# Kernel optimization log

Hardware: AMD Instinct MI355X
Metric: run time of the kernel (lower is better)

The kernel has to match this reference:

```python
import jax, jax.numpy as jnp
import numpy as np

MARGIN = 0.5
TAU = 0.25
RHO = 10.0
SEMIHARD_LOSS_THRESHOLD = 0.0
EPS = 1e-12


def _pairwise_cosine_distances(x):
    # L2-normalize rows, distances = 1 - cosine similarity  -> [N, N]
    xn = x / jnp.maximum(jnp.linalg.norm(x, axis=1, keepdims=True), EPS)
    sim = xn @ xn.T
    dist = 1.0 - sim
    return dist, sim, xn


def _source_similarities(src):
    # distances normalized by their batch mean ('relative' / avg distances)
    dist, sim, xn = _pairwise_cosine_distances(src)
    avg_dist = dist / jnp.maximum(jnp.mean(dist), EPS)
    return dist, avg_dist, sim, xn


def _weights_from_distances(avg_dist, tau):
    # soft relaxed label weights from teacher distances
    pair_weights = jnp.exp(-avg_dist / tau)                      # [N, N] pos-pair weight
    neg_pair_weights = 1.0 - pair_weights                        # [N, N]
    # triplet (i, j=pos, k=neg): weight = w_pos[i,j] * w_neg[i,k]  -> [N, N, N]
    triplet_weights = pair_weights[:, :, None] * neg_pair_weights[:, None, :]
    return pair_weights, neg_pair_weights, triplet_weights


def _safe_division(num, den):
    return jnp.where(den > 0.0, num / jnp.where(den > 0.0, den, 1.0), 0.0)


def setup_inputs() -> dict:
    key = jax.random.key(0)
    k1, k2 = jax.random.split(key)
    N, D = 384, 128
    source_embeddings = jax.random.normal(k1, (N, D), dtype=jnp.float32)
    embeddings = jax.random.normal(k2, (N, D), dtype=jnp.float32)
    return {"source_embeddings": source_embeddings, "embeddings": embeddings}


def reference(source_embeddings, embeddings):
    src = jax.lax.stop_gradient(source_embeddings)  # .detach()
    _, source_avg_distances, _, _ = _source_similarities(src)
    source_pair_weights, _, source_triplet_weights = _weights_from_distances(
        source_avg_distances, TAU)

    distances, _, _ = _pairwise_cosine_distances(embeddings)  # [N, N]
    # tdd[i, j, k] = d[i, k] - d[i, j]
    triplet_distance_differences = distances[:, None, :] - distances[:, :, None]
    triplet_losses = jax.nn.relu(MARGIN - triplet_distance_differences)  # [N, N, N]

    semihard = ((triplet_losses > 0.0) & (triplet_losses <= MARGIN)).astype(
        triplet_losses.dtype) * source_triplet_weights
    positive_pair_semihard_losses = jnp.max(triplet_losses * semihard, axis=2)  # [N, N]

    if SEMIHARD_LOSS_THRESHOLD > 0.0:
        hard = (triplet_losses > MARGIN).astype(triplet_losses.dtype) * source_triplet_weights
        normalized = jnp.min(triplet_losses - RHO * hard, axis=2)
        positive_pair_hard_losses = (normalized + RHO) * (normalized < 0.0).astype(
            normalized.dtype)
    else:
        positive_pair_hard_losses = 0.0

    gate = (positive_pair_semihard_losses <= SEMIHARD_LOSS_THRESHOLD).astype(
        positive_pair_semihard_losses.dtype)
    positive_pair_losses = positive_pair_semihard_losses + gate * positive_pair_hard_losses

    loss = _safe_division(jnp.sum(positive_pair_losses * source_pair_weights),
                          jnp.sum(source_pair_weights))
    return loss
```

## Files before the change

kernel.cpp:

```cpp
#include <hip/hip_runtime.h>
#include <hip/hip_bf16.h>

#define N 384
#define D 128
#define TAU 0.25f
#define MARGIN 0.5f

__global__ __launch_bounds__(64) void k_norm(const float* __restrict__ src,
                                             const float* __restrict__ emb,
                                             float* __restrict__ xn_src,
                                             float* __restrict__ xn_emb,
                                             float* __restrict__ accum) {
    int b = blockIdx.x;
    int lane = threadIdx.x;
    if (b == 0 && lane == 0) { accum[0] = 0.f; accum[1] = 0.f; accum[2] = 0.f; }
    const float* x;
    float* y;
    int row;
    if (b < N) { x = src; y = xn_src; row = b; }
    else       { x = emb; y = xn_emb; row = b - N; }
    float2 v = ((const float2*)(x + (size_t)row * D))[lane];
    float ss = v.x * v.x + v.y * v.y;
    #pragma unroll
    for (int o = 32; o > 0; o >>= 1) ss += __shfl_xor(ss, o);
    float inv = 1.0f / fmaxf(sqrtf(ss), 1e-12f);
    float2 o2 = {v.x * inv, v.y * inv};
    ((float2*)(y + (size_t)row * D))[lane] = o2;
}

__global__ __launch_bounds__(256) void k_gram(const float* __restrict__ xn_src,
                                              const float* __restrict__ xn_emb,
                                              float* __restrict__ dsrc,
                                              float* __restrict__ demb,
                                              float* __restrict__ accum) {
    __shared__ float At[D][34];
    __shared__ float Bt[D][34];
    __shared__ float ps[4];
    int bid = blockIdx.x;
    int mat = (bid >= 144) ? 1 : 0;
    int t2  = mat ? bid - 144 : bid;
    int bi = t2 / 12, bj = t2 % 12;
    const float* xn = mat ? xn_emb : xn_src;
    float* out      = mat ? demb : dsrc;
    int lin = threadIdx.x;
    #pragma unroll
    for (int l = 0; l < 4; l++) {
        int idx = lin + l * 256;
        int row = idx >> 5;
        int c4  = idx & 31;
        float4 va = ((const float4*)(xn + (size_t)(bi * 32 + row) * D))[c4];
        At[c4 * 4 + 0][row] = va.x; At[c4 * 4 + 1][row] = va.y;
        At[c4 * 4 + 2][row] = va.z; At[c4 * 4 + 3][row] = va.w;
        float4 vb = ((const float4*)(xn + (size_t)(bj * 32 + row) * D))[c4];
        Bt[c4 * 4 + 0][row] = vb.x; Bt[c4 * 4 + 1][row] = vb.y;
        Bt[c4 * 4 + 2][row] = vb.z; Bt[c4 * 4 + 3][row] = vb.w;
    }
    __syncthreads();
    int tx = lin & 15, ty = lin >> 4;
    float a00 = 0.f, a01 = 0.f, a10 = 0.f, a11 = 0.f;
    #pragma unroll 8
    for (int k = 0; k < D; k++) {
        float x0 = At[k][2 * ty], x1 = At[k][2 * ty + 1];
        float y0 = Bt[k][2 * tx], y1 = Bt[k][2 * tx + 1];
        a00 = fmaf(x0, y0, a00); a01 = fmaf(x0, y1, a01);
        a10 = fmaf(x1, y0, a10); a11 = fmaf(x1, y1, a11);
    }
    float d00 = 1.f - a00, d01 = 1.f - a01, d10 = 1.f - a10, d11 = 1.f - a11;
    int r0 = bi * 32 + 2 * ty, c0 = bj * 32 + 2 * tx;
    out[(size_t)r0 * N + c0]           = d00;
    out[(size_t)r0 * N + c0 + 1]       = d01;
    out[(size_t)(r0 + 1) * N + c0]     = d10;
    out[(size_t)(r0 + 1) * N + c0 + 1] = d11;
    if (!mat) {
        float s = d00 + d01 + d10 + d11;
        #pragma unroll
        for (int o = 32; o > 0; o >>= 1) s += __shfl_xor(s, o);
        if ((lin & 63) == 0) ps[lin >> 6] = s;
        __syncthreads();
        if (lin == 0) atomicAdd(&accum[0], ps[0] + ps[1] + ps[2] + ps[3]);
    }
}

__global__ __launch_bounds__(256) void k_weights(float* __restrict__ wsrc,
                                                 const float* __restrict__ accum) {
    float mean  = accum[0] * (1.0f / (float)(N * N));
    float scale = 1.0f / (fmaxf(mean, 1e-12f) * TAU);
    int idx = blockIdx.x * 256 + threadIdx.x;
    wsrc[idx] = expf(-wsrc[idx] * scale);
}

__global__ __launch_bounds__(N) void k_main(const float* __restrict__ wp,
                                            const float* __restrict__ de,
                                            float* __restrict__ accum) {
    __shared__ float pn[6], pd[6];
    int i = blockIdx.x;
    int t = threadIdx.x;
    const float* der = de + (size_t)i * N;
    const float* wpr = wp + (size_t)i * N;
    float q = der[t];
    float c = MARGIN + q;
    float m0 = 0.f, m1 = 0.f, m2 = 0.f, m3 = 0.f;
    #pragma unroll 2
    for (int k = 0; k < N; k += 4) {
        float dk0 = der[k], dk1 = der[k + 1], dk2 = der[k + 2], dk3 = der[k + 3];
        float wk0 = wpr[k], wk1 = wpr[k + 1], wk2 = wpr[k + 2], wk3 = wpr[k + 3];
        float tl0 = c - dk0; float v0 = tl0 * (1.f - wk0);
        v0 = (tl0 <= MARGIN) ? v0 : 0.f; m0 = fmaxf(m0, v0);
        float tl1 = c - dk1; float v1 = tl1 * (1.f - wk1);
        v1 = (tl1 <= MARGIN) ? v1 : 0.f; m1 = fmaxf(m1, v1);
        float tl2 = c - dk2; float v2 = tl2 * (1.f - wk2);
        v2 = (tl2 <= MARGIN) ? v2 : 0.f; m2 = fmaxf(m2, v2);
        float tl3 = c - dk3; float v3 = tl3 * (1.f - wk3);
        v3 = (tl3 <= MARGIN) ? v3 : 0.f; m3 = fmaxf(m3, v3);
    }
    float m = fmaxf(fmaxf(m0, m1), fmaxf(m2, m3));
    float w = wpr[t];
    float numc = w * w * m;
    float denc = w;
    #pragma unroll
    for (int o = 32; o > 0; o >>= 1) {
        numc += __shfl_xor(numc, o);
        denc += __shfl_xor(denc, o);
    }
    if ((t & 63) == 0) { pn[t >> 6] = numc; pd[t >> 6] = denc; }
    __syncthreads();
    if (t == 0) {
        float sn = 0.f, sd = 0.f;
        #pragma unroll
        for (int wv = 0; wv < 6; wv++) { sn += pn[wv]; sd += pd[wv]; }
        atomicAdd(&accum[1], sn);
        atomicAdd(&accum[2], sd);
    }
}

__global__ void k_final(const float* __restrict__ accum, float* __restrict__ out) {
    float num = accum[1], den = accum[2];
    out[0] = (den > 0.0f) ? num / den : 0.0f;
}

extern "C" void kernel_launch(void* const* d_in, const int* in_sizes, int n_in,
                              void* d_out, int out_size, void* d_ws, size_t ws_size,
                              hipStream_t stream) {
    const float* src = (const float*)d_in[0];
    const float* emb = (const float*)d_in[1];
    float* out = (float*)d_out;

    float* ws = (float*)d_ws;
    float* xn_src = ws;
    float* xn_emb = xn_src + N * D;
    float* wsrc   = xn_emb + N * D;
    float* demb   = wsrc + N * N;
    float* accum  = demb + N * N;

    k_norm<<<2 * N, 64, 0, stream>>>(src, emb, xn_src, xn_emb, accum);
    k_gram<<<2 * 144, 256, 0, stream>>>(xn_src, xn_emb, wsrc, demb, accum);
    k_weights<<<(N * N) / 256, 256, 0, stream>>>(wsrc, accum);
    k_main<<<N, N, 0, stream>>>(wsrc, demb, accum);
    k_final<<<1, 1, 0, stream>>>(accum, out);
}
```

Baseline: 87.28 us.

## Fuse normalization, weights and final division into two kernels

Row L2 normalization moves into the Gram kernel, where norms are computed per tile and applied while staging into shared memory. The exp weight computation moves into the main kernel, which sums per-block partial distance sums itself. The final division runs in the last block via an atomic ticket counter. This cuts five launches to two and drops intermediate global round-trips, at the cost of redundant norm computation across tiles and a serial 144-element sum in every thread.

```diff
diff --git a/kernel.cpp b/kernel.cpp
--- a/kernel.cpp
+++ b/kernel.cpp
@@ -6,56 +6,57 @@
 #define TAU 0.25f
 #define MARGIN 0.5f
 
-__global__ __launch_bounds__(64) void k_norm(const float* __restrict__ src,
-                                             const float* __restrict__ emb,
-                                             float* __restrict__ xn_src,
-                                             float* __restrict__ xn_emb,
-                                             float* __restrict__ accum) {
-    int b = blockIdx.x;
-    int lane = threadIdx.x;
-    if (b == 0 && lane == 0) { accum[0] = 0.f; accum[1] = 0.f; accum[2] = 0.f; }
-    const float* x;
-    float* y;
-    int row;
-    if (b < N) { x = src; y = xn_src; row = b; }
-    else       { x = emb; y = xn_emb; row = b - N; }
-    float2 v = ((const float2*)(x + (size_t)row * D))[lane];
-    float ss = v.x * v.x + v.y * v.y;
-    #pragma unroll
-    for (int o = 32; o > 0; o >>= 1) ss += __shfl_xor(ss, o);
-    float inv = 1.0f / fmaxf(sqrtf(ss), 1e-12f);
-    float2 o2 = {v.x * inv, v.y * inv};
-    ((float2*)(y + (size_t)row * D))[lane] = o2;
-}
-
-__global__ __launch_bounds__(256) void k_gram(const float* __restrict__ xn_src,
-                                              const float* __restrict__ xn_emb,
+__global__ __launch_bounds__(256) void k_gram(const float* __restrict__ xsrc,
+                                              const float* __restrict__ xemb,
                                               float* __restrict__ dsrc,
                                               float* __restrict__ demb,
+                                              float* __restrict__ tsum,
                                               float* __restrict__ accum) {
     __shared__ float At[D][34];
     __shared__ float Bt[D][34];
+    __shared__ float inv_s[64];
     __shared__ float ps[4];
     int bid = blockIdx.x;
+    int lin = threadIdx.x;
+    if (bid == 0 && lin == 0) {
+        accum[0] = 0.f; accum[1] = 0.f;
+        ((unsigned int*)accum)[2] = 0u;
+    }
     int mat = (bid >= 144) ? 1 : 0;
     int t2  = mat ? bid - 144 : bid;
     int bi = t2 / 12, bj = t2 % 12;
-    const float* xn = mat ? xn_emb : xn_src;
+    const float* xn = mat ? xemb : xsrc;
     float* out      = mat ? demb : dsrc;
-    int lin = threadIdx.x;
+
+    int wv = lin >> 6, lane = lin & 63;
     #pragma unroll
-    for (int l = 0; l < 4; l++) {
+    for (int rr = 0; rr < 16; ++rr) {
+        int vr = wv * 16 + rr;
+        int r  = vr & 31;
+        int grow = ((vr >> 5) ? bj : bi) * 32 + r;
+        float2 v = ((const float2*)(xn + (size_t)grow * D))[lane];
+        float ss = v.x * v.x + v.y * v.y;
+        #pragma unroll
+        for (int o = 32; o > 0; o >>= 1) ss += __shfl_xor(ss, o);
+        if (lane == 0) inv_s[vr] = 1.0f / fmaxf(sqrtf(ss), 1e-12f);
+    }
+    __syncthreads();
+
+    #pragma unroll
+    for (int l = 0; l < 4; ++l) {
         int idx = lin + l * 256;
         int row = idx >> 5;
         int c4  = idx & 31;
+        float ia = inv_s[row], ib = inv_s[32 + row];
         float4 va = ((const float4*)(xn + (size_t)(bi * 32 + row) * D))[c4];
-        At[c4 * 4 + 0][row] = va.x; At[c4 * 4 + 1][row] = va.y;
-        At[c4 * 4 + 2][row] = va.z; At[c4 * 4 + 3][row] = va.w;
+        At[c4 * 4 + 0][row] = va.x * ia; At[c4 * 4 + 1][row] = va.y * ia;
+        At[c4 * 4 + 2][row] = va.z * ia; At[c4 * 4 + 3][row] = va.w * ia;
         float4 vb = ((const float4*)(xn + (size_t)(bj * 32 + row) * D))[c4];
-        Bt[c4 * 4 + 0][row] = vb.x; Bt[c4 * 4 + 1][row] = vb.y;
-        Bt[c4 * 4 + 2][row] = vb.z; Bt[c4 * 4 + 3][row] = vb.w;
+        Bt[c4 * 4 + 0][row] = vb.x * ib; Bt[c4 * 4 + 1][row] = vb.y * ib;
+        Bt[c4 * 4 + 2][row] = vb.z * ib; Bt[c4 * 4 + 3][row] = vb.w * ib;
     }
     __syncthreads();
+
     int tx = lin & 15, ty = lin >> 4;
     float a00 = 0.f, a01 = 0.f, a10 = 0.f, a11 = 0.f;
     #pragma unroll 8
@@ -71,50 +72,52 @@
     out[(size_t)r0 * N + c0 + 1]       = d01;
     out[(size_t)(r0 + 1) * N + c0]     = d10;
     out[(size_t)(r0 + 1) * N + c0 + 1] = d11;
+
     if (!mat) {
         float s = d00 + d01 + d10 + d11;
         #pragma unroll
         for (int o = 32; o > 0; o >>= 1) s += __shfl_xor(s, o);
         if ((lin & 63) == 0) ps[lin >> 6] = s;
         __syncthreads();
-        if (lin == 0) atomicAdd(&accum[0], ps[0] + ps[1] + ps[2] + ps[3]);
+        if (lin == 0) tsum[t2] = ps[0] + ps[1] + ps[2] + ps[3];
     }
 }
 
-__global__ __launch_bounds__(256) void k_weights(float* __restrict__ wsrc,
-                                                 const float* __restrict__ accum) {
-    float mean  = accum[0] * (1.0f / (float)(N * N));
-    float scale = 1.0f / (fmaxf(mean, 1e-12f) * TAU);
-    int idx = blockIdx.x * 256 + threadIdx.x;
-    wsrc[idx] = expf(-wsrc[idx] * scale);
-}
-
-__global__ __launch_bounds__(N) void k_main(const float* __restrict__ wp,
-                                            const float* __restrict__ de,
-                                            float* __restrict__ accum) {
+__global__ __launch_bounds__(N) void k_main(const float* __restrict__ dsrc,
+                                            const float* __restrict__ demb,
+                                            const float* __restrict__ tsum,
+                                            float* __restrict__ accum,
+                                            float* __restrict__ out) {
+    __shared__ float wn[N];
     __shared__ float pn[6], pd[6];
     int i = blockIdx.x;
     int t = threadIdx.x;
-    const float* der = de + (size_t)i * N;
-    const float* wpr = wp + (size_t)i * N;
-    float q = der[t];
-    float c = MARGIN + q;
+    float total = 0.f;
+    #pragma unroll
+    for (int j = 0; j < 144; ++j) total += tsum[j];
+    float mean  = total * (1.0f / (float)(N * N));
+    float scale = 1.0f / (fmaxf(mean, 1e-12f) * TAU);
+    const float* dsr = dsrc + (size_t)i * N;
+    const float* der = demb + (size_t)i * N;
+    float w = expf(-dsr[t] * scale);
+    wn[t] = 1.0f - w;
+    float c = MARGIN + der[t];
+    __syncthreads();
     float m0 = 0.f, m1 = 0.f, m2 = 0.f, m3 = 0.f;
     #pragma unroll 2
     for (int k = 0; k < N; k += 4) {
-        float dk0 = der[k], dk1 = der[k + 1], dk2 = der[k + 2], dk3 = der[k + 3];
-        float wk0 = wpr[k], wk1 = wpr[k + 1], wk2 = wpr[k + 2], wk3 = wpr[k + 3];
-        float tl0 = c - dk0; float v0 = tl0 * (1.f - wk0);
+        float4 wvk = *(const float4*)&wn[k];
+        float d0 = der[k], d1 = der[k + 1], d2 = der[k + 2], d3 = der[k + 3];
+        float tl0 = c - d0; float v0 = tl0 * wvk.x;
         v0 = (tl0 <= MARGIN) ? v0 : 0.f; m0 = fmaxf(m0, v0);
-        float tl1 = c - dk1; float v1 = tl1 * (1.f - wk1);
+        float tl1 = c - d1; float v1 = tl1 * wvk.y;
         v1 = (tl1 <= MARGIN) ? v1 : 0.f; m1 = fmaxf(m1, v1);
-        float tl2 = c - dk2; float v2 = tl2 * (1.f - wk2);
+        float tl2 = c - d2; float v2 = tl2 * wvk.z;
         v2 = (tl2 <= MARGIN) ? v2 : 0.f; m2 = fmaxf(m2, v2);
-        float tl3 = c - dk3; float v3 = tl3 * (1.f - wk3);
+        float tl3 = c - d3; float v3 = tl3 * wvk.w;
         v3 = (tl3 <= MARGIN) ? v3 : 0.f; m3 = fmaxf(m3, v3);
     }
     float m = fmaxf(fmaxf(m0, m1), fmaxf(m2, m3));
-    float w = wpr[t];
     float numc = w * w * m;
     float denc = w;
     #pragma unroll
@@ -128,14 +131,16 @@
         float sn = 0.f, sd = 0.f;
         #pragma unroll
         for (int wv = 0; wv < 6; wv++) { sn += pn[wv]; sd += pd[wv]; }
-        atomicAdd(&accum[1], sn);
-        atomicAdd(&accum[2], sd);
+        atomicAdd(&accum[0], sn);
+        atomicAdd(&accum[1], sd);
+        __threadfence();
+        unsigned int tk = atomicAdd((unsigned int*)accum + 2, 1u);
+        if (tk == (unsigned int)(N - 1)) {
+            float num = atomicAdd(&accum[0], 0.f);
+            float den = atomicAdd(&accum[1], 0.f);
+            out[0] = (den > 0.f) ? num / den : 0.f;
+        }
     }
-}
-
-__global__ void k_final(const float* __restrict__ accum, float* __restrict__ out) {
-    float num = accum[1], den = accum[2];
-    out[0] = (den > 0.0f) ? num / den : 0.0f;
 }
 
 extern "C" void kernel_launch(void* const* d_in, const int* in_sizes, int n_in,
@@ -146,15 +151,11 @@
     float* out = (float*)d_out;
 
     float* ws = (float*)d_ws;
-    float* xn_src = ws;
-    float* xn_emb = xn_src + N * D;
-    float* wsrc   = xn_emb + N * D;
-    float* demb   = wsrc + N * N;
-    float* accum  = demb + N * N;
+    float* dsrc  = ws;
+    float* demb  = dsrc + N * N;
+    float* tsum  = demb + N * N;
+    float* accum = tsum + 144;
 
-    k_norm<<<2 * N, 64, 0, stream>>>(src, emb, xn_src, xn_emb, accum);
-    k_gram<<<2 * 144, 256, 0, stream>>>(xn_src, xn_emb, wsrc, demb, accum);
-    k_weights<<<(N * N) / 256, 256, 0, stream>>>(wsrc, accum);
-    k_main<<<N, N, 0, stream>>>(wsrc, demb, accum);
-    k_final<<<1, 1, 0, stream>>>(accum, out);
+    k_gram<<<288, 256, 0, stream>>>(src, emb, dsrc, demb, tsum, accum);
+    k_main<<<N, N, 0, stream>>>(dsrc, demb, tsum, accum, out);
 }
```

Result: slower. 94.42 us (+8.2%).

## Compute mean distance via column-sum identity and fuse exp into gram kernel

Applied to the files above, without the earlier changes.

Computes the mean source cosine distance algebraically as N^2 minus the squared norm of the summed normalized rows. A small single-block kernel does this before the gram kernel, which lets the exp weight transform be fused into the gram kernel's store and removes the separate weights pass. The final division is folded into the main kernel using a last-block ticket counter, which eliminates the final kernel launch. The net launch count drops from five to four, at the cost of a serial single-block reduction over the 384x128 source matrix.

```diff
diff --git a/kernel.cpp b/kernel.cpp
--- a/kernel.cpp
+++ b/kernel.cpp
@@ -13,7 +13,10 @@
                                              float* __restrict__ accum) {
     int b = blockIdx.x;
     int lane = threadIdx.x;
-    if (b == 0 && lane == 0) { accum[0] = 0.f; accum[1] = 0.f; accum[2] = 0.f; }
+    if (b == 0 && lane == 0) {
+        accum[0] = 0.f; accum[1] = 0.f;
+        ((unsigned int*)accum)[2] = 0u;
+    }
     const float* x;
     float* y;
     int row;
@@ -28,23 +31,53 @@
     ((float2*)(y + (size_t)row * D))[lane] = o2;
 }
 
+__global__ __launch_bounds__(256) void k_scale(const float* __restrict__ xn_src,
+                                               float* __restrict__ accum) {
+    __shared__ float sv[128];
+    __shared__ float ps[2];
+    int t = threadIdx.x;
+    int c = t & 127, h = t >> 7;
+    float s = 0.f;
+    const float* p = xn_src + (size_t)h * 192 * D + c;
+    #pragma unroll 8
+    for (int r = 0; r < 192; ++r) s += p[(size_t)r * D];
+    if (h == 0) sv[c] = s;
+    __syncthreads();
+    if (h == 1) sv[c] += s;
+    __syncthreads();
+    if (t < 128) {
+        float v = sv[t];
+        float sq = v * v;
+        #pragma unroll
+        for (int o = 32; o > 0; o >>= 1) sq += __shfl_xor(sq, o);
+        if ((t & 63) == 0) ps[t >> 6] = sq;
+    }
+    __syncthreads();
+    if (t == 0) {
+        float sum_sim = ps[0] + ps[1];
+        float nn = (float)N * (float)N;
+        float mean = (nn - sum_sim) * (1.0f / nn);
+        accum[3] = 1.0f / (fmaxf(mean, 1e-12f) * TAU);
+    }
+}
+
 __global__ __launch_bounds__(256) void k_gram(const float* __restrict__ xn_src,
                                               const float* __restrict__ xn_emb,
-                                              float* __restrict__ dsrc,
+                                              float* __restrict__ wsrc,
                                               float* __restrict__ demb,
-                                              float* __restrict__ accum) {
+                                              const float* __restrict__ accum) {
     __shared__ float At[D][34];
     __shared__ float Bt[D][34];
-    __shared__ float ps[4];
     int bid = blockIdx.x;
     int mat = (bid >= 144) ? 1 : 0;
     int t2  = mat ? bid - 144 : bid;
     int bi = t2 / 12, bj = t2 % 12;
     const float* xn = mat ? xn_emb : xn_src;
-    float* out      = mat ? demb : dsrc;
+    float* outm     = mat ? demb : wsrc;
+    float scale = accum[3];
     int lin = threadIdx.x;
     #pragma unroll
-    for (int l = 0; l < 4; l++) {
+    for (int l = 0; l < 4; ++l) {
         int idx = lin + l * 256;
         int row = idx >> 5;
         int c4  = idx & 31;
@@ -66,51 +99,39 @@
         a10 = fmaf(x1, y0, a10); a11 = fmaf(x1, y1, a11);
     }
     float d00 = 1.f - a00, d01 = 1.f - a01, d10 = 1.f - a10, d11 = 1.f - a11;
+    if (!mat) {
+        d00 = expf(-d00 * scale); d01 = expf(-d01 * scale);
+        d10 = expf(-d10 * scale); d11 = expf(-d11 * scale);
+    }
     int r0 = bi * 32 + 2 * ty, c0 = bj * 32 + 2 * tx;
-    out[(size_t)r0 * N + c0]           = d00;
-    out[(size_t)r0 * N + c0 + 1]       = d01;
-    out[(size_t)(r0 + 1) * N + c0]     = d10;
-    out[(size_t)(r0 + 1) * N + c0 + 1] = d11;
-    if (!mat) {
-        float s = d00 + d01 + d10 + d11;
-        #pragma unroll
-        for (int o = 32; o > 0; o >>= 1) s += __shfl_xor(s, o);
-        if ((lin & 63) == 0) ps[lin >> 6] = s;
-        __syncthreads();
-        if (lin == 0) atomicAdd(&accum[0], ps[0] + ps[1] + ps[2] + ps[3]);
-    }
+    outm[(size_t)r0 * N + c0]           = d00;
+    outm[(size_t)r0 * N + c0 + 1]       = d01;
+    outm[(size_t)(r0 + 1) * N + c0]     = d10;
+    outm[(size_t)(r0 + 1) * N + c0 + 1] = d11;
 }
 
-__global__ __launch_bounds__(256) void k_weights(float* __restrict__ wsrc,
-                                                 const float* __restrict__ accum) {
-    float mean  = accum[0] * (1.0f / (float)(N * N));
-    float scale = 1.0f / (fmaxf(mean, 1e-12f) * TAU);
-    int idx = blockIdx.x * 256 + threadIdx.x;
-    wsrc[idx] = expf(-wsrc[idx] * scale);
-}
-
-__global__ __launch_bounds__(N) void k_main(const float* __restrict__ wp,
-                                            const float* __restrict__ de,
-                                            float* __restrict__ accum) {
+__global__ __launch_bounds__(N) void k_main(const float* __restrict__ wsrc,
+                                            const float* __restrict__ demb,
+                                            float* __restrict__ accum,
+                                            float* __restrict__ out) {
     __shared__ float pn[6], pd[6];
     int i = blockIdx.x;
     int t = threadIdx.x;
-    const float* der = de + (size_t)i * N;
-    const float* wpr = wp + (size_t)i * N;
-    float q = der[t];
-    float c = MARGIN + q;
+    const float* der = demb + (size_t)i * N;
+    const float* wpr = wsrc + (size_t)i * N;
+    float c = MARGIN + der[t];
     float m0 = 0.f, m1 = 0.f, m2 = 0.f, m3 = 0.f;
     #pragma unroll 2
     for (int k = 0; k < N; k += 4) {
-        float dk0 = der[k], dk1 = der[k + 1], dk2 = der[k + 2], dk3 = der[k + 3];
-        float wk0 = wpr[k], wk1 = wpr[k + 1], wk2 = wpr[k + 2], wk3 = wpr[k + 3];
-        float tl0 = c - dk0; float v0 = tl0 * (1.f - wk0);
+        float d0 = der[k], d1 = der[k + 1], d2 = der[k + 2], d3 = der[k + 3];
+        float w0 = wpr[k], w1 = wpr[k + 1], w2 = wpr[k + 2], w3 = wpr[k + 3];
+        float tl0 = c - d0; float v0 = fmaf(-tl0, w0, tl0);
         v0 = (tl0 <= MARGIN) ? v0 : 0.f; m0 = fmaxf(m0, v0);
-        float tl1 = c - dk1; float v1 = tl1 * (1.f - wk1);
+        float tl1 = c - d1; float v1 = fmaf(-tl1, w1, tl1);
         v1 = (tl1 <= MARGIN) ? v1 : 0.f; m1 = fmaxf(m1, v1);
-        float tl2 = c - dk2; float v2 = tl2 * (1.f - wk2);
+        float tl2 = c - d2; float v2 = fmaf(-tl2, w2, tl2);
         v2 = (tl2 <= MARGIN) ? v2 : 0.f; m2 = fmaxf(m2, v2);
-        float tl3 = c - dk3; float v3 = tl3 * (1.f - wk3);
+        float tl3 = c - d3; float v3 = fmaf(-tl3, w3, tl3);
         v3 = (tl3 <= MARGIN) ? v3 : 0.f; m3 = fmaxf(m3, v3);
     }
     float m = fmaxf(fmaxf(m0, m1), fmaxf(m2, m3));
@@ -128,14 +149,16 @@
         float sn = 0.f, sd = 0.f;
         #pragma unroll
         for (int wv = 0; wv < 6; wv++) { sn += pn[wv]; sd += pd[wv]; }
-        atomicAdd(&accum[1], sn);
-        atomicAdd(&accum[2], sd);
+        atomicAdd(&accum[0], sn);
+        atomicAdd(&accum[1], sd);
+        __threadfence();
+        unsigned tk = atomicAdd((unsigned*)(accum + 2), 1u);
+        if (tk == (unsigned)(N - 1)) {
+            float num = atomicAdd(&accum[0], 0.f);
+            float den = atomicAdd(&accum[1], 0.f);
+            out[0] = (den > 0.f) ? num / den : 0.f;
+        }
     }
-}
-
-__global__ void k_final(const float* __restrict__ accum, float* __restrict__ out) {
-    float num = accum[1], den = accum[2];
-    out[0] = (den > 0.0f) ? num / den : 0.0f;
 }
 
 extern "C" void kernel_launch(void* const* d_in, const int* in_sizes, int n_in,
@@ -153,8 +176,7 @@
     float* accum  = demb + N * N;
 
     k_norm<<<2 * N, 64, 0, stream>>>(src, emb, xn_src, xn_emb, accum);
-    k_gram<<<2 * 144, 256, 0, stream>>>(xn_src, xn_emb, wsrc, demb, accum);
-    k_weights<<<(N * N) / 256, 256, 0, stream>>>(wsrc, accum);
-    k_main<<<N, N, 0, stream>>>(wsrc, demb, accum);
-    k_final<<<1, 1, 0, stream>>>(accum, out);
+    k_scale<<<1, 256, 0, stream>>>(xn_src, accum);
+    k_gram<<<288, 256, 0, stream>>>(xn_src, xn_emb, wsrc, demb, accum);
+    k_main<<<N, N, 0, stream>>>(wsrc, demb, accum, out);
 }
```

Measured after the change: 97.09 us. +11.2%, slower.
